# Kernel tuning notes

Measured on AMD Instinct MI355X. Metric: run time of the kernel, lower is better.

## Reference

```python
import jax, jax.numpy as jnp
import numpy as np

B, N, DIM, H, R = 8, 4096, 256, 8, 32


def setup_inputs() -> dict:
    key = jax.random.key(0)
    k0, k1, k2, k3 = jax.random.split(key, 4)
    x = jax.random.normal(k0, (B, N, DIM), jnp.float32)
    # Dense qkv: in=dim, out=dim*2*num_heads
    qkv_w = jax.random.normal(k1, (DIM, 2 * H * DIM), jnp.float32) * 0.02
    qkv_b = jnp.zeros((2 * H * DIM,), jnp.float32)
    # learned low-rank 'lunchbox' projection (GlorotUniform-ish scale)
    lunchbox = jax.random.normal(k2, (DIM, R), jnp.float32) * (1.0 / np.sqrt(DIM))
    # Dense proj: in=num_heads*dim, out=dim
    proj_w = jax.random.normal(k3, (H * DIM, DIM), jnp.float32) * 0.02
    proj_b = jnp.zeros((DIM,), jnp.float32)
    return dict(x=x, qkv_w=qkv_w, qkv_b=qkv_b, lunchbox=lunchbox,
                proj_w=proj_w, proj_b=proj_b)


def reference(x, qkv_w, qkv_b, lunchbox, proj_w, proj_b):
    Bsz, Nseq, C = x.shape
    D, Rr = lunchbox.shape            # (dim, lunchbox_dim)
    Hh = qkv_w.shape[1] // (2 * D)    # num_heads
    scale = max(D, Rr) ** -0.5

    h = x @ qkv_w + qkv_b                                   # (B, N, 2*H*D)
    h = jnp.transpose(h, (0, 2, 1)).reshape(Bsz, 2, Hh, D, Nseq)
    q, v = h[:, 0], h[:, 1]                                 # (B, H, D, N)

    # einsum('bikj,kr->birk'): reduce over sequence j, keep dim k elementwise
    attn = jnp.einsum('bhdn,dr->bhrd', q, lunchbox) * scale  # (B, H, R, D)
    # NOTE: original TF code calls tf.nn.softmax(attn, -1) but DISCARDS the
    # result (unassigned) -- faithfully reproduced as a no-op here.

    # einsum('birk,bikn->bink'): reduce over lunchbox rank r
    res = jnp.einsum('bhrd,bhdn->bhnd', attn, v)             # (B, H, N, D)

    # raw reshape (NOT a transpose), exactly as in the TF source
    out = res.reshape(Bsz, Nseq, Hh * D) @ proj_w + proj_b   # (B, N, dim)
    return out
```

## Files before the change

kernel.cpp:

```cpp
#include <hip/hip_runtime.h>
#include <stdint.h>

typedef unsigned short u16;
typedef unsigned int u32;
typedef __attribute__((ext_vector_type(8))) short short8;
typedef __attribute__((ext_vector_type(4))) float f32x4;

#define B_    8
#define N_    4096
#define DIM_  256
#define HD_   2048
#define NQKV_ 4096

__device__ __forceinline__ float bf2f(u16 u) {
  union { u32 u; float f; } v; v.u = ((u32)u) << 16; return v.f;
}
__device__ __forceinline__ u16 f2bf(float f) {
  union { float f; u32 u; } v; v.f = f;
  u32 r = v.u + 0x7fffu + ((v.u >> 16) & 1u);
  return (u16)(r >> 16);
}
__device__ __forceinline__ float ldin(const void* p, size_t i, int isbf) {
  return isbf ? bf2f(((const u16*)p)[i]) : ((const float*)p)[i];
}
__device__ __forceinline__ void load16_to_lds(const u16* gsrc, u16* ldst) {
  auto gp = (const __attribute__((address_space(1))) void*)(uintptr_t)gsrc;
  auto lp = (__attribute__((address_space(3))) void*)(uintptr_t)ldst;
  __builtin_amdgcn_global_load_lds(gp, lp, 16, 0, 0);
}
__device__ __forceinline__ int probe_isbf(const void* x) {
  u32 w = ((const u32*)x)[threadIdx.x & 63];
  int e = (int)((w >> 7) & 0xff);
  unsigned long long m = __ballot(e >= 118 && e <= 130);
  return __popcll(m) >= 32;
}

__global__ void cvtsum_kernel(const void* __restrict__ x, u16* __restrict__ xb,
                              float* __restrict__ part) {
  int isbf = probe_isbf(x);
  int b = blockIdx.x >> 7, ch = blockIdx.x & 127, t = threadIdx.x;
  size_t base = ((size_t)b * N_ + (size_t)ch * 32) * DIM_ + t;
  float s = 0.f;
  for (int n = 0; n < 32; ++n) {
    float v = ldin(x, base + (size_t)n * DIM_, isbf);
    xb[base + (size_t)n * DIM_] = f2bf(v);
    s += v;
  }
  part[(b * 128 + ch) * DIM_ + t] = s;
}

__global__ void prep_kernel(const void* __restrict__ x, const void* __restrict__ qkv_w,
                            const void* __restrict__ proj_w, const void* __restrict__ qkv_b,
                            const void* __restrict__ proj_b, const void* __restrict__ lunchbox,
                            u16* __restrict__ wv, u16* __restrict__ pt,
                            float* __restrict__ Psum, float* __restrict__ qb,
                            float* __restrict__ pbv, float* __restrict__ Lsum,
                            const float* __restrict__ part, float* __restrict__ xsum) {
  int isbf = probe_isbf(x);
  int bid = blockIdx.x, t = threadIdx.x;
  if (bid < 256) {
    size_t i = ((size_t)bid * 256 + t) * 8;
    int k = (int)(i >> 11), e = (int)(i & 2047);
    size_t src = (size_t)k * NQKV_ + HD_ + e;
    short8 o;
#pragma unroll
    for (int j = 0; j < 8; ++j) o[j] = (short)f2bf(ldin(qkv_w, src + j, isbf));
    *(short8*)&wv[i] = o;
  } else if (bid < 768) {
    __shared__ float tile[32][33];
    int bid2 = bid - 256;
    int c0 = (bid2 & 7) * 32, e0 = (bid2 >> 3) * 32;
    int tx = t & 31, ty = t >> 5;
    for (int i = ty; i < 32; i += 8)
      tile[i][tx] = ldin(proj_w, (size_t)(e0 + i) * 256 + c0 + tx, isbf);
    __syncthreads();
    for (int i = ty; i < 32; i += 8)
      pt[(size_t)(c0 + i) * HD_ + e0 + tx] = f2bf(tile[tx][i]);
  } else if (bid < 1024) {
    int d = bid - 768;
    float s = 0.f;
    for (int jj = 0; jj < 8; ++jj) s += ldin(proj_w, (size_t)(jj * 256 + d) * 256 + t, isbf);
    Psum[d * 256 + t] = s;
  } else if (bid < 1040) {
    int i = (bid - 1024) * 256 + t;
    qb[i] = ldin(qkv_b, i, isbf);
  } else if (bid == 1040) {
    pbv[t] = ldin(proj_b, t, isbf);
  } else if (bid == 1041) {
    float s = 0.f;
    for (int r = 0; r < 32; ++r) s += ldin(lunchbox, (size_t)t * 32 + r, isbf);
    Lsum[t] = s;
  } else {
    int b = bid - 1042;
    float s = 0.f;
    for (int c = 0; c < 128; ++c) s += part[(b * 128 + c) * DIM_ + t];
    xsum[b * DIM_ + t] = s;
  }
}

__global__ void gpart_kernel(const void* __restrict__ xraw, const void* __restrict__ qkv_w,
                             const float* __restrict__ xsum, float* __restrict__ gpart) {
  int isbf = probe_isbf(xraw);
  int bid = blockIdx.x, t = threadIdx.x;
  int kc = bid & 3, hc = (bid >> 2) & 7, b = bid >> 5;
  __shared__ float xs[64];
  if (t < 64) xs[t] = xsum[b * 256 + kc * 64 + t];
  __syncthreads();
  int hd = hc * 256 + t;
  float s = 0.f;
#pragma unroll 8
  for (int i = 0; i < 64; ++i)
    s += xs[i] * ldin(qkv_w, (size_t)(kc * 64 + i) * NQKV_ + hd, isbf);
  gpart[kc * 16384 + b * HD_ + hd] = s;
}

__global__ void gfin_kernel(const float* __restrict__ gpart, const float* __restrict__ qb,
                            const float* __restrict__ Lsum, const float* __restrict__ Psum,
                            float* __restrict__ g, float* __restrict__ rcpart) {
  int bid = blockIdx.x, t = threadIdx.x;
  int ds = bid & 3, bh = bid >> 2;
  int b = bh >> 3, h = bh & 7;
  __shared__ float us[64];
  if (t < 64) {
    int d = ds * 64 + t, hd = h * 256 + d;
    float sum = gpart[b * HD_ + hd] + gpart[16384 + b * HD_ + hd] +
                gpart[32768 + b * HD_ + hd] + gpart[49152 + b * HD_ + hd];
    float gg = 0.0625f * (sum + 4096.0f * qb[hd]) * Lsum[d];
    g[b * HD_ + hd] = gg;
    us[t] = gg * qb[HD_ + hd];
  }
  __syncthreads();
  float r = 0.f;
#pragma unroll 8
  for (int i = 0; i < 64; ++i)
    r += us[i] * Psum[(ds * 64 + i) * 256 + t];
  rcpart[ds * 16384 + bh * 256 + t] = r;
}

__global__ __launch_bounds__(256, 2) void stage1_kernel(
    const u16* __restrict__ pt, const u16* __restrict__ wv,
    const float* __restrict__ g, u16* __restrict__ Mt, int b0) {
  __shared__ alignas(16) char smem[81920];
  u16* Wp = (u16*)smem;
  char* Adb = smem + 65536;
  float* eps = (float*)(smem + 65536);

  int bid = blockIdx.x;
  int c0i = bid & 1, jh = (bid >> 1) & 1, k0i = (bid >> 2) & 1;
  int h = (bid >> 3) & 7, bb = bid >> 6;
  int b = b0 + bb;
  int c0 = c0i * 128, k0 = k0i * 128;
  const int t = threadIdx.x, lane = t & 63, wave = t >> 6;
  const int wr = wave >> 1, wc = wave & 1;
  const int panel = bb * 8 + h;

  {
    const u16* wsrc = wv + (size_t)k0 * HD_ + h * 256;
    const float* gp = g + b * HD_ + h * 256;
#pragma unroll
    for (int it = 0; it < 16; ++it) {
      int idx = it * 256 + t;
      int row = idx >> 5, chunk = idx & 31;
      short8 w8 = *(const short8*)&wsrc[(size_t)row * HD_ + chunk * 8];
      f32x4 g0 = *(const f32x4*)&gp[chunk * 8];
      f32x4 g1 = *(const f32x4*)&gp[chunk * 8 + 4];
      short8 o;
      o[0] = (short)f2bf(bf2f((u16)w8[0]) * g0[0]);
      o[1] = (short)f2bf(bf2f((u16)w8[1]) * g0[1]);
      o[2] = (short)f2bf(bf2f((u16)w8[2]) * g0[2]);
      o[3] = (short)f2bf(bf2f((u16)w8[3]) * g0[3]);
      o[4] = (short)f2bf(bf2f((u16)w8[4]) * g1[0]);
      o[5] = (short)f2bf(bf2f((u16)w8[5]) * g1[1]);
      o[6] = (short)f2bf(bf2f((u16)w8[6]) * g1[2]);
      o[7] = (short)f2bf(bf2f((u16)w8[7]) * g1[3]);
      *(short8*)&Wp[row * 256 + ((chunk ^ (row & 7)) * 8)] = o;
    }
  }
  __syncthreads();

#define S1_STAGE(jj, ks, bi)                                                          \
  {                                                                                   \
    _Pragma("unroll") for (int it = 0; it < 2; ++it) {                                \
      int idx = it * 256 + t, row = idx >> 2, slot = idx & 3;                         \
      load16_to_lds(pt + (size_t)(c0 + row) * HD_ + (jj) * 256 + (ks) * 32 +          \
                        ((slot ^ (row & 3)) * 8),                                     \
                    (u16*)(Adb + (bi) * 8192) + idx * 8);                             \
    }                                                                                 \
  }

  for (int jc = 0; jc < 4; ++jc) {
    int jj = jh * 4 + jc;
    f32x4 acc[4][4] = {};
    S1_STAGE(jj, 0, 0);
    __syncthreads();
    int cur = 0;
    for (int ks = 0; ks < 8; ++ks) {
      if (ks < 7) S1_STAGE(jj, ks + 1, cur ^ 1);
      const u16* lA = (const u16*)(Adb + cur * 8192);
      short8 af[4], bfr[4];
      const int ar = wr * 64 + (lane & 15), bc = wc * 64 + (lane & 15);
#pragma unroll
      for (int mi = 0; mi < 4; ++mi) {
        int row = ar + mi * 16;
        af[mi] = *(const short8*)&lA[row * 32 + (((lane >> 4) ^ (row & 3)) * 8)];
      }
#pragma unroll
      for (int ni = 0; ni < 4; ++ni) {
        int kl = bc + ni * 16;
        int chunk = ks * 4 + (lane >> 4);
        bfr[ni] = *(const short8*)&Wp[kl * 256 + ((chunk ^ (kl & 7)) * 8)];
      }
#pragma unroll
      for (int mi = 0; mi < 4; ++mi)
#pragma unroll
        for (int ni = 0; ni < 4; ++ni)
          acc[mi][ni] = __builtin_amdgcn_mfma_f32_16x16x32_bf16(af[mi], bfr[ni], acc[mi][ni], 0, 0, 0);
      __syncthreads();
      cur ^= 1;
    }
    const int rl = t >> 3, cc = (t & 7) * 16;
#pragma unroll
    for (int mi = 0; mi < 4; ++mi) {
      __syncthreads();
#pragma unroll
      for (int ni = 0; ni < 4; ++ni) {
        f32x4 v = acc[mi][ni];
        int re = wr * 16 + (lane >> 4) * 4, ce = wc * 64 + ni * 16 + (lane & 15);
        eps[(re + 0) * 128 + ce] = v[0];
        eps[(re + 1) * 128 + ce] = v[1];
        eps[(re + 2) * 128 + ce] = v[2];
        eps[(re + 3) * 128 + ce] = v[3];
      }
      __syncthreads();
      int cg = c0 + (rl >> 4) * 64 + mi * 16 + (rl & 15);
      alignas(16) u16 pk[16];
#pragma unroll
      for (int j = 0; j < 16; ++j) pk[j] = f2bf(eps[rl * 128 + cc + j]);
      u16* dst = Mt + (size_t)panel * 524288 + (size_t)cg * HD_ + jj * 256 + k0 + cc;
      *(short8*)dst = *(short8*)pk;
      *(short8*)(dst + 8) = *(short8*)(pk + 8);
    }
    __syncthreads();
  }
}

__global__ __launch_bounds__(512, 4) void stage2_kernel(
    const void* __restrict__ xraw, const u16* __restrict__ xb, const u16* __restrict__ Mt,
    const float* __restrict__ rcpart, const float* __restrict__ pbv,
    void* __restrict__ outv, int b0, int nblk) {
  __shared__ alignas(16) char smem[65536];
  float* eps = (float*)smem;

  int bid = blockIdx.x;
  int sid = (bid & 7) * (nblk >> 3) + (bid >> 3);
  int ct = sid & 1, rt = (sid >> 1) & 3, h = (sid >> 3) & 7, bb = sid >> 6;
  int b = b0 + bb;
  int nn0 = rt * 128, c0 = ct * 128;
  const int panel = bb * 8 + h;
  const u16* Abase = xb + (size_t)b * 1048576 + (size_t)nn0 * HD_;
  const u16* Bbase = Mt + (size_t)panel * 524288 + (size_t)c0 * HD_;

  const int t = threadIdx.x;
  const int grp = t >> 8, tt = t & 255;
  const int lane = tt & 63, wave = tt >> 6;
  const int wr = wave >> 1, wc = wave & 1;
  char* mybuf = smem + grp * 32768;

  f32x4 acc[4][4] = {};

#define S2_STAGE(i, bi)                                                            \
  {                                                                                \
    int kcol = ((i) * 2 + grp) * 32;                                               \
    _Pragma("unroll") for (int it = 0; it < 2; ++it) {                             \
      int idx = it * 256 + tt, row = idx >> 2, slot = idx & 3;                     \
      int sc = kcol + ((slot ^ (row & 3)) * 8);                                    \
      load16_to_lds(Abase + (size_t)row * HD_ + sc,                                \
                    (u16*)(mybuf + (bi) * 16384) + idx * 8);                       \
      load16_to_lds(Bbase + (size_t)row * HD_ + sc,                                \
                    (u16*)(mybuf + (bi) * 16384 + 8192) + idx * 8);                \
    }                                                                              \
  }

  S2_STAGE(0, 0);
  __syncthreads();
  int cur = 0;
  for (int i = 0; i < 32; ++i) {
    if (i < 31) S2_STAGE(i + 1, cur ^ 1);
    const u16* lA = (const u16*)(mybuf + cur * 16384);
    const u16* lB = lA + 4096;
    short8 af[4], bfr[4];
    const int ar = wr * 64 + (lane & 15), bc = wc * 64 + (lane & 15);
#pragma unroll
    for (int mi = 0; mi < 4; ++mi) {
      int row = ar + mi * 16;
      af[mi] = *(const short8*)&lA[row * 32 + (((lane >> 4) ^ (row & 3)) * 8)];
    }
#pragma unroll
    for (int ni = 0; ni < 4; ++ni) {
      int row = bc + ni * 16;
      bfr[ni] = *(const short8*)&lB[row * 32 + (((lane >> 4) ^ (row & 3)) * 8)];
    }
#pragma unroll
    for (int mi = 0; mi < 4; ++mi)
#pragma unroll
      for (int ni = 0; ni < 4; ++ni)
        acc[mi][ni] = __builtin_amdgcn_mfma_f32_16x16x32_bf16(af[mi], bfr[ni], acc[mi][ni], 0, 0, 0);
    __syncthreads();
    cur ^= 1;
  }

  int isbf = probe_isbf(xraw);
  const int rl = t >> 4, cc = (t & 15) * 8;
  float rc[8];
  {
    const float* rp = rcpart + (size_t)(b * 8 + h) * 256 + c0 + cc;
    const float* pb = pbv + c0 + cc;
#pragma unroll
    for (int j = 0; j < 8; ++j)
      rc[j] = rp[j] + rp[16384 + j] + rp[32768 + j] + rp[49152 + j] + pb[j];
  }
#pragma unroll
  for (int mi = 0; mi < 4; ++mi) {
    __syncthreads();
    if (grp == 0) {
#pragma unroll
      for (int ni = 0; ni < 4; ++ni) {
        f32x4 v = acc[mi][ni];
        int re = wr * 16 + (lane >> 4) * 4, ce = wc * 64 + ni * 16 + (lane & 15);
        eps[(re + 0) * 128 + ce] = v[0];
        eps[(re + 1) * 128 + ce] = v[1];
        eps[(re + 2) * 128 + ce] = v[2];
        eps[(re + 3) * 128 + ce] = v[3];
      }
    }
    __syncthreads();
    if (grp == 1) {
#pragma unroll
      for (int ni = 0; ni < 4; ++ni) {
        f32x4 v = acc[mi][ni];
        int re = wr * 16 + (lane >> 4) * 4, ce = wc * 64 + ni * 16 + (lane & 15);
        eps[(re + 0) * 128 + ce] += v[0];
        eps[(re + 1) * 128 + ce] += v[1];
        eps[(re + 2) * 128 + ce] += v[2];
        eps[(re + 3) * 128 + ce] += v[3];
      }
    }
    __syncthreads();
    int grow = b * N_ + h * 512 + nn0 + (rl >> 4) * 64 + mi * 16 + (rl & 15);
    if (isbf) {
      alignas(16) u16 pk[8];
#pragma unroll
      for (int j = 0; j < 8; ++j) pk[j] = f2bf(eps[rl * 128 + cc + j] + rc[j]);
      *(short8*)((u16*)outv + (size_t)grow * 256 + c0 + cc) = *(short8*)pk;
    } else {
      float* op = (float*)outv + (size_t)grow * 256 + c0 + cc;
      f32x4 o0, o1;
      o0[0] = eps[rl * 128 + cc + 0] + rc[0];
      o0[1] = eps[rl * 128 + cc + 1] + rc[1];
      o0[2] = eps[rl * 128 + cc + 2] + rc[2];
      o0[3] = eps[rl * 128 + cc + 3] + rc[3];
      o1[0] = eps[rl * 128 + cc + 4] + rc[4];
      o1[1] = eps[rl * 128 + cc + 5] + rc[5];
      o1[2] = eps[rl * 128 + cc + 6] + rc[6];
      o1[3] = eps[rl * 128 + cc + 7] + rc[7];
      ((f32x4*)op)[0] = o0;
      ((f32x4*)op)[1] = o1;
    }
  }
}

extern "C" void kernel_launch(void* const* d_in, const int* in_sizes, int n_in,
                              void* d_out, int out_size, void* d_ws, size_t ws_size,
                              hipStream_t stream) {
  const void* x        = d_in[0];
  const void* qkv_w    = d_in[1];
  const void* qkv_b    = d_in[2];
  const void* lunchbox = d_in[3];
  const void* proj_w   = d_in[4];
  const void* proj_b   = d_in[5];
  char* ws = (char*)d_ws;

  u16*   xbuf   = (u16*)(ws + 0);
  u16*   wv     = (u16*)(ws + 16777216);
  u16*   pt     = (u16*)(ws + 17825792);
  float* part   = (float*)(ws + 18874368);
  float* xsum   = (float*)(ws + 19922944);
  float* g      = (float*)(ws + 19931136);
  float* gpart  = (float*)(ws + 19996672);
  float* rcpart = (float*)(ws + 20258816);
  float* Psum   = (float*)(ws + 20520960);
  float* qb     = (float*)(ws + 20783104);
  float* pbv    = (float*)(ws + 20799488);
  float* Lsum   = (float*)(ws + 20800512);
  u16*   Mt     = (u16*)(ws + 20971520);

  cvtsum_kernel<<<1024, 256, 0, stream>>>(x, xbuf, part);
  prep_kernel<<<1050, 256, 0, stream>>>(x, qkv_w, proj_w, qkv_b, proj_b, lunchbox,
                                        wv, pt, Psum, qb, pbv, Lsum, part, xsum);
  gpart_kernel<<<256, 256, 0, stream>>>(x, qkv_w, xsum, gpart);
  gfin_kernel<<<256, 256, 0, stream>>>(gpart, qb, Lsum, Psum, g, rcpart);

  size_t mt_off = 20971520;
  int gb = 8;
  while (gb > 1 && mt_off + (size_t)gb * 8388608 > ws_size) gb >>= 1;
  for (int b0 = 0; b0 < 8; b0 += gb) {
    stage1_kernel<<<gb * 64, 256, 0, stream>>>(pt, wv, g, Mt, b0);
    int nblk = gb * 64;
    stage2_kernel<<<nblk, 512, 0, stream>>>(x, xbuf, Mt, rcpart, pbv, d_out, b0, nblk);
  }
}
```

Measured before the change: 104.2 us.

## Restructure stage2 GEMM to 128x256 tiles with 5-stage LDS pipeline; vectorize cvtsum

```diff
diff --git a/kernel.cpp b/kernel.cpp
--- a/kernel.cpp
+++ b/kernel.cpp
@@ -39,14 +39,38 @@
                               float* __restrict__ part) {
   int isbf = probe_isbf(x);
   int b = blockIdx.x >> 7, ch = blockIdx.x & 127, t = threadIdx.x;
-  size_t base = ((size_t)b * N_ + (size_t)ch * 32) * DIM_ + t;
-  float s = 0.f;
-  for (int n = 0; n < 32; ++n) {
-    float v = ldin(x, base + (size_t)n * DIM_, isbf);
-    xb[base + (size_t)n * DIM_] = f2bf(v);
-    s += v;
-  }
-  part[(b * 128 + ch) * DIM_ + t] = s;
+  int c8 = (t & 31) * 8, rg = t >> 5;
+  __shared__ float sm[8][256];
+  float s[8] = {0.f, 0.f, 0.f, 0.f, 0.f, 0.f, 0.f, 0.f};
+#pragma unroll
+  for (int i = 0; i < 4; ++i) {
+    int row = rg * 4 + i;
+    size_t off = ((size_t)b * N_ + (size_t)ch * 32 + row) * DIM_ + c8;
+    if (isbf) {
+      short8 v = *(const short8*)((const u16*)x + off);
+      *(short8*)(xb + off) = v;
+#pragma unroll
+      for (int j = 0; j < 8; ++j) s[j] += bf2f((u16)v[j]);
+    } else {
+      f32x4 a = *(const f32x4*)((const float*)x + off);
+      f32x4 bb = *(const f32x4*)((const float*)x + off + 4);
+      short8 o;
+      o[0] = (short)f2bf(a[0]); o[1] = (short)f2bf(a[1]);
+      o[2] = (short)f2bf(a[2]); o[3] = (short)f2bf(a[3]);
+      o[4] = (short)f2bf(bb[0]); o[5] = (short)f2bf(bb[1]);
+      o[6] = (short)f2bf(bb[2]); o[7] = (short)f2bf(bb[3]);
+      *(short8*)(xb + off) = o;
+      s[0] += a[0]; s[1] += a[1]; s[2] += a[2]; s[3] += a[3];
+      s[4] += bb[0]; s[5] += bb[1]; s[6] += bb[2]; s[7] += bb[3];
+    }
+  }
+#pragma unroll
+  for (int j = 0; j < 8; ++j) sm[rg][c8 + j] = s[j];
+  __syncthreads();
+  float tot = 0.f;
+#pragma unroll
+  for (int r = 0; r < 8; ++r) tot += sm[r][t];
+  part[(b * 128 + ch) * DIM_ + t] = tot;
 }
 
 __global__ void prep_kernel(const void* __restrict__ x, const void* __restrict__ qkv_w,
@@ -244,127 +268,131 @@
   }
 }
 
-__global__ __launch_bounds__(512, 4) void stage2_kernel(
+__global__ __launch_bounds__(512, 1) void stage2_kernel(
     const void* __restrict__ xraw, const u16* __restrict__ xb, const u16* __restrict__ Mt,
     const float* __restrict__ rcpart, const float* __restrict__ pbv,
     void* __restrict__ outv, int b0, int nblk) {
-  __shared__ alignas(16) char smem[65536];
+  __shared__ alignas(16) char smem[122880];
   float* eps = (float*)smem;
 
   int bid = blockIdx.x;
   int sid = (bid & 7) * (nblk >> 3) + (bid >> 3);
-  int ct = sid & 1, rt = (sid >> 1) & 3, h = (sid >> 3) & 7, bb = sid >> 6;
+  int mblk = sid & 3, h = (sid >> 2) & 7, bb = sid >> 5;
   int b = b0 + bb;
-  int nn0 = rt * 128, c0 = ct * 128;
+  int nn0 = mblk * 128;
   const int panel = bb * 8 + h;
   const u16* Abase = xb + (size_t)b * 1048576 + (size_t)nn0 * HD_;
-  const u16* Bbase = Mt + (size_t)panel * 524288 + (size_t)c0 * HD_;
-
-  const int t = threadIdx.x;
-  const int grp = t >> 8, tt = t & 255;
-  const int lane = tt & 63, wave = tt >> 6;
-  const int wr = wave >> 1, wc = wave & 1;
-  char* mybuf = smem + grp * 32768;
+  const u16* Bbase = Mt + (size_t)panel * 524288;
+
+  const int t = threadIdx.x, lane = t & 63, wave = t >> 6;
+  const int wr = wave >> 2, wc = wave & 3;
 
   f32x4 acc[4][4] = {};
 
-#define S2_STAGE(i, bi)                                                            \
-  {                                                                                \
-    int kcol = ((i) * 2 + grp) * 32;                                               \
-    _Pragma("unroll") for (int it = 0; it < 2; ++it) {                             \
-      int idx = it * 256 + tt, row = idx >> 2, slot = idx & 3;                     \
-      int sc = kcol + ((slot ^ (row & 3)) * 8);                                    \
-      load16_to_lds(Abase + (size_t)row * HD_ + sc,                                \
-                    (u16*)(mybuf + (bi) * 16384) + idx * 8);                       \
-      load16_to_lds(Bbase + (size_t)row * HD_ + sc,                                \
-                    (u16*)(mybuf + (bi) * 16384 + 8192) + idx * 8);                \
-    }                                                                              \
-  }
-
-  S2_STAGE(0, 0);
-  __syncthreads();
+#define S2_STAGE(kt_, cb_)                                                          \
+  {                                                                                 \
+    int kcol = (kt_) * 32;                                                          \
+    {                                                                               \
+      int row = t >> 2, slot = t & 3;                                               \
+      load16_to_lds(Abase + (size_t)row * HD_ + kcol + ((slot ^ ((row >> 1) & 3)) * 8), \
+                    (u16*)(cb_) + t * 8);                                           \
+    }                                                                               \
+    _Pragma("unroll") for (int qi = 0; qi < 2; ++qi) {                              \
+      int q2 = qi * 512 + t;                                                        \
+      int row = q2 >> 2, slot = q2 & 3;                                             \
+      load16_to_lds(Bbase + (size_t)row * HD_ + kcol + ((slot ^ ((row >> 1) & 3)) * 8), \
+                    (u16*)(cb_) + 4096 + q2 * 8);                                   \
+    }                                                                               \
+  }
+
+#pragma unroll
+  for (int i = 0; i < 5; ++i) S2_STAGE(i, smem + i * 24576);
+  asm volatile("s_waitcnt vmcnt(12)" ::: "memory");
+  __builtin_amdgcn_s_barrier();
+  __builtin_amdgcn_sched_barrier(0);
+
   int cur = 0;
-  for (int i = 0; i < 32; ++i) {
-    if (i < 31) S2_STAGE(i + 1, cur ^ 1);
-    const u16* lA = (const u16*)(mybuf + cur * 16384);
-    const u16* lB = lA + 4096;
+  for (int kt = 0; kt < 64; ++kt) {
+    char* cb = smem + cur * 24576;
+    const u16* lA = (const u16*)cb;
+    const u16* lB = (const u16*)(cb + 8192);
     short8 af[4], bfr[4];
-    const int ar = wr * 64 + (lane & 15), bc = wc * 64 + (lane & 15);
 #pragma unroll
     for (int mi = 0; mi < 4; ++mi) {
-      int row = ar + mi * 16;
-      af[mi] = *(const short8*)&lA[row * 32 + (((lane >> 4) ^ (row & 3)) * 8)];
+      int row = wr * 64 + mi * 16 + (lane & 15);
+      af[mi] = *(const short8*)&lA[row * 32 + (((lane >> 4) ^ ((row >> 1) & 3)) * 8)];
     }
 #pragma unroll
     for (int ni = 0; ni < 4; ++ni) {
-      int row = bc + ni * 16;
-      bfr[ni] = *(const short8*)&lB[row * 32 + (((lane >> 4) ^ (row & 3)) * 8)];
-    }
+      int row = wc * 64 + ni * 16 + (lane & 15);
+      bfr[ni] = *(const short8*)&lB[row * 32 + (((lane >> 4) ^ ((row >> 1) & 3)) * 8)];
+    }
+    __builtin_amdgcn_s_setprio(1);
 #pragma unroll
     for (int mi = 0; mi < 4; ++mi)
 #pragma unroll
       for (int ni = 0; ni < 4; ++ni)
         acc[mi][ni] = __builtin_amdgcn_mfma_f32_16x16x32_bf16(af[mi], bfr[ni], acc[mi][ni], 0, 0, 0);
-    __syncthreads();
-    cur ^= 1;
+    __builtin_amdgcn_s_setprio(0);
+    asm volatile("" ::: "memory");
+    __builtin_amdgcn_sched_barrier(0);
+    __builtin_amdgcn_s_barrier();
+    if (kt < 59) S2_STAGE(kt + 5, cb);
+    if (kt <= 58)      { asm volatile("s_waitcnt vmcnt(12)" ::: "memory"); }
+    else if (kt == 59) { asm volatile("s_waitcnt vmcnt(9)" ::: "memory"); }
+    else if (kt == 60) { asm volatile("s_waitcnt vmcnt(6)" ::: "memory"); }
+    else if (kt == 61) { asm volatile("s_waitcnt vmcnt(3)" ::: "memory"); }
+    else if (kt == 62) { asm volatile("s_waitcnt vmcnt(0)" ::: "memory"); }
+    if (kt < 63) {
+      __builtin_amdgcn_s_barrier();
+      asm volatile("" ::: "memory");
+      __builtin_amdgcn_sched_barrier(0);
+    }
+    cur = (cur == 4) ? 0 : cur + 1;
   }
 
   int isbf = probe_isbf(xraw);
-  const int rl = t >> 4, cc = (t & 15) * 8;
-  float rc[8];
+  const int rl = t >> 4, cc = (t & 15) * 16;
+  float rc[16];
   {
-    const float* rp = rcpart + (size_t)(b * 8 + h) * 256 + c0 + cc;
-    const float* pb = pbv + c0 + cc;
-#pragma unroll
-    for (int j = 0; j < 8; ++j)
+    const float* rp = rcpart + (size_t)(b * 8 + h) * 256 + cc;
+    const float* pb = pbv + cc;
+#pragma unroll
+    for (int j = 0; j < 16; ++j)
       rc[j] = rp[j] + rp[16384 + j] + rp[32768 + j] + rp[49152 + j] + pb[j];
   }
 #pragma unroll
   for (int mi = 0; mi < 4; ++mi) {
     __syncthreads();
-    if (grp == 0) {
-#pragma unroll
-      for (int ni = 0; ni < 4; ++ni) {
-        f32x4 v = acc[mi][ni];
-        int re = wr * 16 + (lane >> 4) * 4, ce = wc * 64 + ni * 16 + (lane & 15);
-        eps[(re + 0) * 128 + ce] = v[0];
-        eps[(re + 1) * 128 + ce] = v[1];
-        eps[(re + 2) * 128 + ce] = v[2];
-        eps[(re + 3) * 128 + ce] = v[3];
-      }
-    }
-    __syncthreads();
-    if (grp == 1) {
-#pragma unroll
-      for (int ni = 0; ni < 4; ++ni) {
-        f32x4 v = acc[mi][ni];
-        int re = wr * 16 + (lane >> 4) * 4, ce = wc * 64 + ni * 16 + (lane & 15);
-        eps[(re + 0) * 128 + ce] += v[0];
-        eps[(re + 1) * 128 + ce] += v[1];
-        eps[(re + 2) * 128 + ce] += v[2];
-        eps[(re + 3) * 128 + ce] += v[3];
-      }
+#pragma unroll
+    for (int ni = 0; ni < 4; ++ni) {
+      f32x4 v = acc[mi][ni];
+      int re = wr * 16 + (lane >> 4) * 4, ce = wc * 64 + ni * 16 + (lane & 15);
+      eps[(re + 0) * 256 + ce] = v[0];
+      eps[(re + 1) * 256 + ce] = v[1];
+      eps[(re + 2) * 256 + ce] = v[2];
+      eps[(re + 3) * 256 + ce] = v[3];
     }
     __syncthreads();
     int grow = b * N_ + h * 512 + nn0 + (rl >> 4) * 64 + mi * 16 + (rl & 15);
     if (isbf) {
-      alignas(16) u16 pk[8];
-#pragma unroll
-      for (int j = 0; j < 8; ++j) pk[j] = f2bf(eps[rl * 128 + cc + j] + rc[j]);
-      *(short8*)((u16*)outv + (size_t)grow * 256 + c0 + cc) = *(short8*)pk;
+      alignas(16) u16 pk[16];
+#pragma unroll
+      for (int j = 0; j < 16; ++j) pk[j] = f2bf(eps[rl * 256 + cc + j] + rc[j]);
+      u16* op = (u16*)outv + (size_t)grow * 256 + cc;
+      *(short8*)op = *(short8*)pk;
+      *(short8*)(op + 8) = *(short8*)(pk + 8);
     } else {
-      float* op = (float*)outv + (size_t)grow * 256 + c0 + cc;
-      f32x4 o0, o1;
-      o0[0] = eps[rl * 128 + cc + 0] + rc[0];
-      o0[1] = eps[rl * 128 + cc + 1] + rc[1];
-      o0[2] = eps[rl * 128 + cc + 2] + rc[2];
-      o0[3] = eps[rl * 128 + cc + 3] + rc[3];
-      o1[0] = eps[rl * 128 + cc + 4] + rc[4];
-      o1[1] = eps[rl * 128 + cc + 5] + rc[5];
-      o1[2] = eps[rl * 128 + cc + 6] + rc[6];
-      o1[3] = eps[rl * 128 + cc + 7] + rc[7];
-      ((f32x4*)op)[0] = o0;
-      ((f32x4*)op)[1] = o1;
+      float* op = (float*)outv + (size_t)grow * 256 + cc;
+#pragma unroll
+      for (int ch = 0; ch < 4; ++ch) {
+        f32x4 o_;
+        o_[0] = eps[rl * 256 + cc + ch * 4 + 0] + rc[ch * 4 + 0];
+        o_[1] = eps[rl * 256 + cc + ch * 4 + 1] + rc[ch * 4 + 1];
+        o_[2] = eps[rl * 256 + cc + ch * 4 + 2] + rc[ch * 4 + 2];
+        o_[3] = eps[rl * 256 + cc + ch * 4 + 3] + rc[ch * 4 + 3];
+        ((f32x4*)op)[ch] = o_;
+      }
     }
   }
 }
@@ -405,7 +433,7 @@
   while (gb > 1 && mt_off + (size_t)gb * 8388608 > ws_size) gb >>= 1;
   for (int b0 = 0; b0 < 8; b0 += gb) {
     stage1_kernel<<<gb * 64, 256, 0, stream>>>(pt, wv, g, Mt, b0);
-    int nblk = gb * 64;
+    int nblk = gb * 32;
     stage2_kernel<<<nblk, 512, 0, stream>>>(x, xbuf, Mt, rcpart, pbv, d_out, b0, nblk);
   }
 }
```

Measured after the change: 112.2 us. 7.6% more time.

## Load stage2 B operand directly to registers, halve LDS, vectorize cvtsum, reswizzle

Applied to the files above, without the earlier changes.

```diff
diff --git a/kernel.cpp b/kernel.cpp
--- a/kernel.cpp
+++ b/kernel.cpp
@@ -39,14 +39,38 @@
                               float* __restrict__ part) {
   int isbf = probe_isbf(x);
   int b = blockIdx.x >> 7, ch = blockIdx.x & 127, t = threadIdx.x;
-  size_t base = ((size_t)b * N_ + (size_t)ch * 32) * DIM_ + t;
-  float s = 0.f;
-  for (int n = 0; n < 32; ++n) {
-    float v = ldin(x, base + (size_t)n * DIM_, isbf);
-    xb[base + (size_t)n * DIM_] = f2bf(v);
-    s += v;
-  }
-  part[(b * 128 + ch) * DIM_ + t] = s;
+  int c8 = (t & 31) * 8, rg = t >> 5;
+  __shared__ float sm[8][256];
+  float s[8] = {0.f, 0.f, 0.f, 0.f, 0.f, 0.f, 0.f, 0.f};
+#pragma unroll
+  for (int i = 0; i < 4; ++i) {
+    int row = rg * 4 + i;
+    size_t off = ((size_t)b * N_ + (size_t)ch * 32 + row) * DIM_ + c8;
+    if (isbf) {
+      short8 v = *(const short8*)((const u16*)x + off);
+      *(short8*)(xb + off) = v;
+#pragma unroll
+      for (int j = 0; j < 8; ++j) s[j] += bf2f((u16)v[j]);
+    } else {
+      f32x4 a = *(const f32x4*)((const float*)x + off);
+      f32x4 bb = *(const f32x4*)((const float*)x + off + 4);
+      short8 o;
+      o[0] = (short)f2bf(a[0]); o[1] = (short)f2bf(a[1]);
+      o[2] = (short)f2bf(a[2]); o[3] = (short)f2bf(a[3]);
+      o[4] = (short)f2bf(bb[0]); o[5] = (short)f2bf(bb[1]);
+      o[6] = (short)f2bf(bb[2]); o[7] = (short)f2bf(bb[3]);
+      *(short8*)(xb + off) = o;
+      s[0] += a[0]; s[1] += a[1]; s[2] += a[2]; s[3] += a[3];
+      s[4] += bb[0]; s[5] += bb[1]; s[6] += bb[2]; s[7] += bb[3];
+    }
+  }
+#pragma unroll
+  for (int j = 0; j < 8; ++j) sm[rg][c8 + j] = s[j];
+  __syncthreads();
+  float tot = 0.f;
+#pragma unroll
+  for (int r = 0; r < 8; ++r) tot += sm[r][t];
+  part[(b * 128 + ch) * DIM_ + t] = tot;
 }
 
 __global__ void prep_kernel(const void* __restrict__ x, const void* __restrict__ qkv_w,
@@ -183,7 +207,7 @@
     _Pragma("unroll") for (int it = 0; it < 2; ++it) {                                \
       int idx = it * 256 + t, row = idx >> 2, slot = idx & 3;                         \
       load16_to_lds(pt + (size_t)(c0 + row) * HD_ + (jj) * 256 + (ks) * 32 +          \
-                        ((slot ^ (row & 3)) * 8),                                     \
+                        ((slot ^ ((row >> 1) & 3)) * 8),                              \
                     (u16*)(Adb + (bi) * 8192) + idx * 8);                             \
     }                                                                                 \
   }
@@ -202,7 +226,7 @@
 #pragma unroll
       for (int mi = 0; mi < 4; ++mi) {
         int row = ar + mi * 16;
-        af[mi] = *(const short8*)&lA[row * 32 + (((lane >> 4) ^ (row & 3)) * 8)];
+        af[mi] = *(const short8*)&lA[row * 32 + (((lane >> 4) ^ ((row >> 1) & 3)) * 8)];
       }
 #pragma unroll
       for (int ni = 0; ni < 4; ++ni) {
@@ -248,7 +272,7 @@
     const void* __restrict__ xraw, const u16* __restrict__ xb, const u16* __restrict__ Mt,
     const float* __restrict__ rcpart, const float* __restrict__ pbv,
     void* __restrict__ outv, int b0, int nblk) {
-  __shared__ alignas(16) char smem[65536];
+  __shared__ alignas(16) char smem[32768];
   float* eps = (float*)smem;
 
   int bid = blockIdx.x;
@@ -264,49 +288,58 @@
   const int grp = t >> 8, tt = t & 255;
   const int lane = tt & 63, wave = tt >> 6;
   const int wr = wave >> 1, wc = wave & 1;
-  char* mybuf = smem + grp * 32768;
+  char* aB0 = smem + grp * 16384;
+  char* aB1 = aB0 + 8192;
 
   f32x4 acc[4][4] = {};
-
-#define S2_STAGE(i, bi)                                                            \
-  {                                                                                \
-    int kcol = ((i) * 2 + grp) * 32;                                               \
-    _Pragma("unroll") for (int it = 0; it < 2; ++it) {                             \
-      int idx = it * 256 + tt, row = idx >> 2, slot = idx & 3;                     \
-      int sc = kcol + ((slot ^ (row & 3)) * 8);                                    \
-      load16_to_lds(Abase + (size_t)row * HD_ + sc,                                \
-                    (u16*)(mybuf + (bi) * 16384) + idx * 8);                       \
-      load16_to_lds(Bbase + (size_t)row * HD_ + sc,                                \
-                    (u16*)(mybuf + (bi) * 16384 + 8192) + idx * 8);                \
-    }                                                                              \
-  }
-
-  S2_STAGE(0, 0);
+  short8 bX[4], bY[4];
+
+#define S2_STAGE_A(i_, dst_)                                                        \
+  {                                                                                 \
+    int kcol = ((i_) * 2 + grp) * 32;                                               \
+    _Pragma("unroll") for (int it = 0; it < 2; ++it) {                              \
+      int idx = it * 256 + tt, row = idx >> 2, slot = idx & 3;                      \
+      load16_to_lds(Abase + (size_t)row * HD_ + kcol + ((slot ^ ((row >> 1) & 3)) * 8), \
+                    (u16*)(dst_) + idx * 8);                                        \
+    }                                                                               \
+  }
+#define S2_LOADB(breg_, i_)                                                         \
+  {                                                                                 \
+    int kcol = ((i_) * 2 + grp) * 32;                                               \
+    _Pragma("unroll") for (int ni = 0; ni < 4; ++ni)                                \
+      breg_[ni] = *(const short8*)(Bbase +                                          \
+          (size_t)(wc * 64 + ni * 16 + (lane & 15)) * HD_ + kcol + (lane >> 4) * 8);\
+  }
+#define S2_COMP(buf_, breg_)                                                        \
+  {                                                                                 \
+    const u16* lA = (const u16*)(buf_);                                             \
+    short8 af[4];                                                                   \
+    _Pragma("unroll") for (int mi = 0; mi < 4; ++mi) {                              \
+      int row = wr * 64 + mi * 16 + (lane & 15);                                    \
+      af[mi] = *(const short8*)&lA[row * 32 + (((lane >> 4) ^ ((row >> 1) & 3)) * 8)]; \
+    }                                                                               \
+    _Pragma("unroll") for (int mi = 0; mi < 4; ++mi)                                \
+      _Pragma("unroll") for (int ni = 0; ni < 4; ++ni)                              \
+        acc[mi][ni] = __builtin_amdgcn_mfma_f32_16x16x32_bf16(af[mi], breg_[ni],    \
+                                                              acc[mi][ni], 0, 0, 0);\
+  }
+
+  S2_STAGE_A(0, aB0);
+  S2_LOADB(bX, 0);
   __syncthreads();
-  int cur = 0;
-  for (int i = 0; i < 32; ++i) {
-    if (i < 31) S2_STAGE(i + 1, cur ^ 1);
-    const u16* lA = (const u16*)(mybuf + cur * 16384);
-    const u16* lB = lA + 4096;
-    short8 af[4], bfr[4];
-    const int ar = wr * 64 + (lane & 15), bc = wc * 64 + (lane & 15);
-#pragma unroll
-    for (int mi = 0; mi < 4; ++mi) {
-      int row = ar + mi * 16;
-      af[mi] = *(const short8*)&lA[row * 32 + (((lane >> 4) ^ (row & 3)) * 8)];
-    }
-#pragma unroll
-    for (int ni = 0; ni < 4; ++ni) {
-      int row = bc + ni * 16;
-      bfr[ni] = *(const short8*)&lB[row * 32 + (((lane >> 4) ^ (row & 3)) * 8)];
-    }
-#pragma unroll
-    for (int mi = 0; mi < 4; ++mi)
-#pragma unroll
-      for (int ni = 0; ni < 4; ++ni)
-        acc[mi][ni] = __builtin_amdgcn_mfma_f32_16x16x32_bf16(af[mi], bfr[ni], acc[mi][ni], 0, 0, 0);
-    __syncthreads();
-    cur ^= 1;
+#pragma unroll 1
+  for (int ii = 0; ii < 16; ++ii) {
+    int i0 = ii * 2;
+    S2_STAGE_A(i0 + 1, aB1);
+    S2_LOADB(bY, i0 + 1);
+    S2_COMP(aB0, bX);
+    __syncthreads();
+    if (ii < 15) {
+      S2_STAGE_A(i0 + 2, aB0);
+      S2_LOADB(bX, i0 + 2);
+    }
+    S2_COMP(aB1, bY);
+    __syncthreads();
   }
 
   int isbf = probe_isbf(xraw);
```

New measurement: 137.9 us. 32.3% more time.
